# Optimization experiments

Hardware: AMD Instinct MI355X
Metric: run time of the kernel (lower is better)

## Reference

```python
import jax, jax.numpy as jnp
import numpy as np

B, T, D = 2, 2048, 1024
H, KVH = 16, 4
HD = D // H            # 64
E, TOPK, FFH = 8, 2, 2048
EPS = 1e-6
ROPE_THETA = 10000.0


def rmsnorm(x, w):
    return x * jax.lax.rsqrt(jnp.mean(x * x, axis=-1, keepdims=True) + EPS) * w


def rope(x, cos, sin):
    # x: (B, h, T, hd); pairs (even, odd) treated as complex, matching view_as_complex
    x2 = x.reshape(*x.shape[:-1], -1, 2)
    x0, x1 = x2[..., 0], x2[..., 1]
    o0 = x0 * cos - x1 * sin
    o1 = x0 * sin + x1 * cos
    return jnp.stack([o0, o1], axis=-1).reshape(x.shape)


def setup_inputs() -> dict:
    key = jax.random.key(0)
    ks = jax.random.split(key, 12)
    s = 0.02
    return {
        'x': jax.random.normal(ks[0], (B, T, D), dtype=jnp.float32),
        'attn_norm_w': jnp.ones((D,), jnp.float32),
        'wq': jax.random.normal(ks[1], (D, H * HD), jnp.float32) * s,
        'wk': jax.random.normal(ks[2], (D, KVH * HD), jnp.float32) * s,
        'wv': jax.random.normal(ks[3], (D, KVH * HD), jnp.float32) * s,
        'wo': jax.random.normal(ks[4], (D, D), jnp.float32) * s,
        'ffn_norm_w': jnp.ones((D,), jnp.float32),
        'gate_w': jax.random.normal(ks[5], (D, E), jnp.float32) * s,
        'gate_bias': jnp.zeros((E,), jnp.float32),  # e_score_correction_bias (aux-loss-free)
        'expert_w1': jax.random.normal(ks[6], (E, D, FFH), jnp.float32) * s,
        'expert_w2': jax.random.normal(ks[7], (E, FFH, D), jnp.float32) * s,
        'shared_w1': jax.random.normal(ks[8], (D, FFH), jnp.float32) * s,
        'shared_w2': jax.random.normal(ks[9], (FFH, D), jnp.float32) * s,
    }


def block_forward(x, attn_norm_w, wq, wk, wv, wo, ffn_norm_w, gate_w, gate_bias,
                  expert_w1, expert_w2, shared_w1, shared_w2):
    # ---- RoPE tables (precompute_freqs_cis, scaling_factor=1.0) ----
    half = HD // 2
    inv_freq = 1.0 / (ROPE_THETA ** (jnp.arange(half, dtype=jnp.float32) / half))
    t = jnp.arange(T, dtype=jnp.float32)
    fr = t[:, None] * inv_freq          # (T, half)
    cos, sin = jnp.cos(fr), jnp.sin(fr)

    # ---- attn_norm + GQA attention ----
    h = rmsnorm(x, attn_norm_w)
    q = (h @ wq).reshape(B, T, H, HD).transpose(0, 2, 1, 3)      # (B,H,T,HD)
    k = (h @ wk).reshape(B, T, KVH, HD).transpose(0, 2, 1, 3)    # (B,KVH,T,HD)
    v = (h @ wv).reshape(B, T, KVH, HD).transpose(0, 2, 1, 3)
    q = rope(q, cos, sin)
    k = rope(k, cos, sin)
    n_rep = H // KVH
    k = jnp.repeat(k, n_rep, axis=1)    # repeat_interleave over head dim
    v = jnp.repeat(v, n_rep, axis=1)
    att = jnp.einsum('bhqd,bhkd->bhqk', q, k) * (HD ** -0.5)
    causal = jnp.tril(jnp.ones((T, T), dtype=bool))
    att = jnp.where(causal, att, jnp.finfo(att.dtype).min)
    att = jax.nn.softmax(att, axis=-1)
    attn_out = jnp.einsum('bhqk,bhkd->bhqd', att, v).transpose(0, 2, 1, 3).reshape(B, T, D) @ wo
    x1 = x + attn_out

    # ---- ffn_norm + MoE feed-forward ----
    h2 = rmsnorm(x1, ffn_norm_w).reshape(-1, D)                  # (N, D)
    N = B * T
    shared = jax.nn.silu(h2 @ shared_w1) @ shared_w2             # 1 shared expert
    scores = jax.nn.sigmoid(h2 @ gate_w) + gate_bias             # sigmoid gate + correction bias
    topk_w, topk_i = jax.lax.top_k(scores, TOPK)
    topk_w = topk_w / (topk_w.sum(-1, keepdims=True) + 1e-20)    # norm_topk_prob; routed_scale=1.0
    combine = jnp.zeros((N, E), x.dtype).at[jnp.arange(N)[:, None], topk_i].add(topk_w)
    hmid = jax.nn.silu(jnp.einsum('nd,edh->enh', h2, expert_w1)) # (E,N,FFH)
    eout = jnp.einsum('enh,ehd->end', hmid, expert_w2)           # (E,N,D)
    routed = jnp.einsum('end,ne->nd', eout, combine)
    return x1 + (shared + routed).reshape(B, T, D)


def reference(x, attn_norm_w, wq, wk, wv, wo, ffn_norm_w, gate_w, gate_bias,
              expert_w1, expert_w2, shared_w1, shared_w2):
    return block_forward(x, attn_norm_w, wq, wk, wv, wo, ffn_norm_w, gate_w, gate_bias,
                         expert_w1, expert_w2, shared_w1, shared_w2)
```

## Files before the change

### kernel.cpp

```cpp
#include <hip/hip_runtime.h>
#include <math.h>

#define NTOK 4096
#define DM 1024
#define TSEQ 2048
#define NH 16
#define NKV 4
#define HDIM 64
#define NE 8
#define NFF 2048
#define QKVN 1536

typedef float f4v __attribute__((ext_vector_type(4)));
typedef short b8v __attribute__((ext_vector_type(8)));
typedef unsigned short u16;

__device__ __forceinline__ float silu_f(float v) { return v / (1.0f + expf(-v)); }

__device__ __forceinline__ u16 f2b(float f) {
    union { float f; unsigned u; } x{f};
    unsigned r = (x.u + 0x7FFFu + ((x.u >> 16) & 1u)) >> 16;
    return (u16)r;
}
__device__ __forceinline__ float b2f(u16 b) {
    union { unsigned u; float f; } x;
    x.u = ((unsigned)b) << 16;
    return x.f;
}

template <int MODE>
__global__ __launch_bounds__(256) void rmsnorm2_k(const float* __restrict__ x,
                                                  const float* __restrict__ w,
                                                  u16* __restrict__ oh, u16* __restrict__ ol,
                                                  float* __restrict__ of) {
    int row = blockIdx.x;
    int tid = threadIdx.x;
    const float4 v = ((const float4*)(x + (size_t)row * DM))[tid];
    float ss = v.x * v.x + v.y * v.y + v.z * v.z + v.w * v.w;
    for (int off = 32; off; off >>= 1) ss += __shfl_down(ss, off);
    __shared__ float red[4];
    if ((tid & 63) == 0) red[tid >> 6] = ss;
    __syncthreads();
    float tot = red[0] + red[1] + red[2] + red[3];
    float inv = rsqrtf(tot * (1.0f / DM) + 1e-6f);
    const float4 wv = ((const float4*)w)[tid];
    float o[4];
    o[0] = v.x * inv * wv.x; o[1] = v.y * inv * wv.y;
    o[2] = v.z * inv * wv.z; o[3] = v.w * inv * wv.w;
    if (MODE == 1) {
        float4 f; f.x = o[0]; f.y = o[1]; f.z = o[2]; f.w = o[3];
        ((float4*)(of + (size_t)row * DM))[tid] = f;
        ushort4 hb;
        hb.x = f2b(o[0]); hb.y = f2b(o[1]); hb.z = f2b(o[2]); hb.w = f2b(o[3]);
        ((ushort4*)(oh + (size_t)row * DM))[tid] = hb;
    } else {
        ushort4 hb, lb;
#pragma unroll
        for (int i = 0; i < 4; ++i) {
            u16 h = f2b(o[i]);
            u16 l = f2b(o[i] - b2f(h));
            ((u16*)&hb)[i] = h;
            ((u16*)&lb)[i] = l;
        }
        ((ushort4*)(oh + (size_t)row * DM))[tid] = hb;
        ((ushort4*)(ol + (size_t)row * DM))[tid] = lb;
    }
}

__global__ __launch_bounds__(256) void scast_k(const float* __restrict__ in, int stride,
                                               int colbase, int cols,
                                               u16* __restrict__ oh, u16* __restrict__ ol) {
    int idx = blockIdx.x * 256 + threadIdx.x;
    int cpr = cols >> 3;
    int row = idx / cpr;
    int cc = (idx - row * cpr) << 3;
    const float* p = in + (size_t)row * stride + colbase + cc;
    const float4 a = *(const float4*)p;
    const float4 b = *(const float4*)(p + 4);
    float vv[8] = {a.x, a.y, a.z, a.w, b.x, b.y, b.z, b.w};
    ushort4 h0, h1, l0, l1;
#pragma unroll
    for (int i = 0; i < 8; ++i) {
        u16 h = f2b(vv[i]);
        u16 l = f2b(vv[i] - b2f(h));
        if (i < 4) { ((u16*)&h0)[i] = h; ((u16*)&l0)[i] = l; }
        else       { ((u16*)&h1)[i - 4] = h; ((u16*)&l1)[i - 4] = l; }
    }
    u16* po = oh + (size_t)row * cols + cc;
    u16* pl = ol + (size_t)row * cols + cc;
    *(ushort4*)po = h0; *(ushort4*)(po + 4) = h1;
    *(ushort4*)pl = l0; *(ushort4*)(pl + 4) = l1;
}

__global__ __launch_bounds__(256) void vtrans_k(const float* __restrict__ qkv,
                                                u16* __restrict__ oh, u16* __restrict__ ol) {
    __shared__ float tl[32][33];
    int c0 = blockIdx.x << 5;
    int r0 = blockIdx.y << 5;
    int lr = threadIdx.x >> 3, lc = (threadIdx.x & 7) << 2;
    const float4 v = *(const float4*)&qkv[(size_t)(r0 + lr) * QKVN + 1280 + c0 + lc];
    tl[lr][lc] = v.x; tl[lr][lc + 1] = v.y; tl[lr][lc + 2] = v.z; tl[lr][lc + 3] = v.w;
    __syncthreads();
    int b = r0 >> 11;
    size_t obase = ((size_t)(b * 256 + c0 + lr)) * TSEQ + (r0 & 2047) + lc;
    ushort4 h4, l4;
#pragma unroll
    for (int i = 0; i < 4; ++i) {
        float f = tl[lc + i][lr];
        u16 h = f2b(f);
        u16 l = f2b(f - b2f(h));
        ((u16*)&h4)[i] = h; ((u16*)&l4)[i] = l;
    }
    *(ushort4*)&oh[obase] = h4;
    *(ushort4*)&ol[obase] = l4;
}

__global__ __launch_bounds__(256) void tcast2_k(const float* __restrict__ in,
                                                u16* __restrict__ oh, u16* __restrict__ ol,
                                                int R, int C) {
    __shared__ float tl[32][33];
    int r0 = blockIdx.y << 5, c0 = blockIdx.x << 5;
    int lr = threadIdx.x >> 3, lc = (threadIdx.x & 7) << 2;
    const float4 v = *(const float4*)&in[(size_t)(r0 + lr) * C + c0 + lc];
    tl[lr][lc] = v.x; tl[lr][lc + 1] = v.y; tl[lr][lc + 2] = v.z; tl[lr][lc + 3] = v.w;
    __syncthreads();
    ushort4 h4, l4;
#pragma unroll
    for (int i = 0; i < 4; ++i) {
        float f = tl[lc + i][lr];
        u16 h = f2b(f);
        u16 l = f2b(f - b2f(h));
        ((u16*)&h4)[i] = h; ((u16*)&l4)[i] = l;
    }
    size_t ob = (size_t)(c0 + lr) * R + r0 + lc;
    *(ushort4*)&oh[ob] = h4;
    *(ushort4*)&ol[ob] = l4;
}

__global__ __launch_bounds__(256) void tcast_k(const float* __restrict__ in,
                                               u16* __restrict__ out, int R, int C) {
    size_t boff = (size_t)blockIdx.z * R * C;
    in += boff; out += boff;
    __shared__ float tl[32][33];
    int r0 = blockIdx.y << 5, c0 = blockIdx.x << 5;
    int lr = threadIdx.x >> 3, lc = (threadIdx.x & 7) << 2;
    const float4 v = *(const float4*)&in[(size_t)(r0 + lr) * C + c0 + lc];
    tl[lr][lc] = v.x; tl[lr][lc + 1] = v.y; tl[lr][lc + 2] = v.z; tl[lr][lc + 3] = v.w;
    __syncthreads();
    ushort4 o;
    o.x = f2b(tl[lc + 0][lr]); o.y = f2b(tl[lc + 1][lr]);
    o.z = f2b(tl[lc + 2][lr]); o.w = f2b(tl[lc + 3][lr]);
    *(ushort4*)&out[(size_t)(c0 + lr) * R + r0 + lc] = o;
}

__global__ void rope2_k(float* __restrict__ x, int nheads, int colbase) {
    int idx = blockIdx.x * blockDim.x + threadIdx.x;
    int total = NTOK * nheads * 32;
    if (idx >= total) return;
    int j = idx & 31;
    int hh = (idx >> 5) % nheads;
    int n = idx / (nheads * 32);
    int t = n & (TSEQ - 1);
    float inv = expf(-(float)j * (0.03125f * logf(10000.0f)));
    float s, c;
    sincosf((float)t * inv, &s, &c);
    float* p = x + (size_t)n * QKVN + colbase + hh * 64 + j * 2;
    float x0 = p[0], x1 = p[1];
    p[0] = x0 * c - x1 * s;
    p[1] = x0 * s + x1 * c;
}

template <int EPI>
__global__ __launch_bounds__(256) void sgemm_k(const u16* __restrict__ Ah,
                                               const u16* __restrict__ Al,
                                               const u16* __restrict__ Bh,
                                               const u16* __restrict__ Bl,
                                               const float* __restrict__ Rr,
                                               float* __restrict__ C,
                                               int M, int N, int K) {
    __shared__ u16 Ash[128 * 40], Asl[128 * 40], Bsh[128 * 40], Bsl[128 * 40];
    int t = threadIdx.x;
    int l = t & 63, w = t >> 6;
    int wr = w >> 1, wc = w & 1;
    int n0 = blockIdx.x * 128, m0 = blockIdx.y * 128;
    int srow = t >> 2, scol = (t & 3) << 3;
    const u16 *agh[2], *agl[2], *bgh[2], *bgl[2];
#pragma unroll
    for (int i = 0; i < 2; ++i) {
        size_t ao = (size_t)(m0 + i * 64 + srow) * K + scol;
        size_t bo = (size_t)(n0 + i * 64 + srow) * K + scol;
        agh[i] = Ah + ao; agl[i] = Al + ao;
        bgh[i] = Bh + bo; bgl[i] = Bl + bo;
    }
    f4v acc[4][4];
#pragma unroll
    for (int m = 0; m < 4; ++m)
#pragma unroll
        for (int n = 0; n < 4; ++n) acc[m][n] = (f4v)0.0f;
    int kh_ = (l >> 4) << 3;
    for (int k0 = 0; k0 < K; k0 += 32) {
        b8v vah0 = *(const b8v*)(agh[0] + k0);
        b8v vah1 = *(const b8v*)(agh[1] + k0);
        b8v val0 = *(const b8v*)(agl[0] + k0);
        b8v val1 = *(const b8v*)(agl[1] + k0);
        b8v vbh0 = *(const b8v*)(bgh[0] + k0);
        b8v vbh1 = *(const b8v*)(bgh[1] + k0);
        b8v vbl0 = *(const b8v*)(bgl[0] + k0);
        b8v vbl1 = *(const b8v*)(bgl[1] + k0);
        __syncthreads();
        *(b8v*)&Ash[srow * 40 + scol] = vah0;
        *(b8v*)&Ash[(64 + srow) * 40 + scol] = vah1;
        *(b8v*)&Asl[srow * 40 + scol] = val0;
        *(b8v*)&Asl[(64 + srow) * 40 + scol] = val1;
        *(b8v*)&Bsh[srow * 40 + scol] = vbh0;
        *(b8v*)&Bsh[(64 + srow) * 40 + scol] = vbh1;
        *(b8v*)&Bsl[srow * 40 + scol] = vbl0;
        *(b8v*)&Bsl[(64 + srow) * 40 + scol] = vbl1;
        __syncthreads();
        b8v afh[4], afl[4], bfh[4], bfl[4];
#pragma unroll
        for (int m = 0; m < 4; ++m) {
            int ro = (wr * 64 + m * 16 + (l & 15)) * 40 + kh_;
            afh[m] = *(const b8v*)&Ash[ro];
            afl[m] = *(const b8v*)&Asl[ro];
        }
#pragma unroll
        for (int n = 0; n < 4; ++n) {
            int ro = (wc * 64 + n * 16 + (l & 15)) * 40 + kh_;
            bfh[n] = *(const b8v*)&Bsh[ro];
            bfl[n] = *(const b8v*)&Bsl[ro];
        }
#pragma unroll
        for (int m = 0; m < 4; ++m)
#pragma unroll
            for (int n = 0; n < 4; ++n) {
                acc[m][n] = __builtin_amdgcn_mfma_f32_16x16x32_bf16(afl[m], bfh[n], acc[m][n], 0, 0, 0);
                acc[m][n] = __builtin_amdgcn_mfma_f32_16x16x32_bf16(afh[m], bfl[n], acc[m][n], 0, 0, 0);
                acc[m][n] = __builtin_amdgcn_mfma_f32_16x16x32_bf16(afh[m], bfh[n], acc[m][n], 0, 0, 0);
            }
    }
#pragma unroll
    for (int m = 0; m < 4; ++m) {
        int r0l = m0 + wr * 64 + m * 16 + ((l >> 4) << 2);
#pragma unroll
        for (int n = 0; n < 4; ++n) {
            int col = n0 + wc * 64 + n * 16 + (l & 15);
            f4v c = acc[m][n];
#pragma unroll
            for (int j = 0; j < 4; ++j) {
                size_t idx = (size_t)(r0l + j) * N + col;
                float v = c[j];
                if (EPI == 2) v += Rr[idx];
                C[idx] = v;
            }
        }
    }
}

__global__ __launch_bounds__(256) void mattn_k(const u16* __restrict__ qh, const u16* __restrict__ ql,
                                               const u16* __restrict__ kh, const u16* __restrict__ kl,
                                               const u16* __restrict__ vth, const u16* __restrict__ vtl,
                                               float* __restrict__ o) {
    __shared__ u16 plds[4][2][16][72];
    int t = threadIdx.x, l = t & 63, w = t >> 6;
    int bh = blockIdx.y, b = bh >> 4, h = bh & 15, kvh = h >> 2;
    int q0 = blockIdx.x * 64;
    size_t bT = (size_t)b * TSEQ;
    int lx = l & 15, lg = l >> 4;
    b8v qfh[2], qfl[2];
    {
        size_t qo = (bT + q0 + w * 16 + lx) * DM + h * 64 + lg * 8;
        qfh[0] = *(const b8v*)(qh + qo);
        qfh[1] = *(const b8v*)(qh + qo + 32);
        qfl[0] = *(const b8v*)(ql + qo);
        qfl[1] = *(const b8v*)(ql + qo + 32);
    }
    f4v acc[4];
#pragma unroll
    for (int ht = 0; ht < 4; ++ht) acc[ht] = (f4v)0.0f;
    float m_r[4], l_r[4];
    int qg[4];
#pragma unroll
    for (int r = 0; r < 4; ++r) {
        m_r[r] = -3.0e38f; l_r[r] = 0.0f;
        qg[r] = q0 + w * 16 + lg * 4 + r;
    }
    int ntile = (q0 >> 6) + 1;
    for (int kt = 0; kt < ntile; ++kt) {
        int kv0 = kt << 6;
        f4v s[4];
#pragma unroll
        for (int st = 0; st < 4; ++st) {
            size_t ko = (bT + kv0 + st * 16 + lx) * 256 + kvh * 64 + lg * 8;
            b8v kf0h = *(const b8v*)(kh + ko);
            b8v kf1h = *(const b8v*)(kh + ko + 32);
            b8v kf0l = *(const b8v*)(kl + ko);
            b8v kf1l = *(const b8v*)(kl + ko + 32);
            f4v ss = (f4v)0.0f;
            ss = __builtin_amdgcn_mfma_f32_16x16x32_bf16(qfl[0], kf0h, ss, 0, 0, 0);
            ss = __builtin_amdgcn_mfma_f32_16x16x32_bf16(qfh[0], kf0l, ss, 0, 0, 0);
            ss = __builtin_amdgcn_mfma_f32_16x16x32_bf16(qfh[0], kf0h, ss, 0, 0, 0);
            ss = __builtin_amdgcn_mfma_f32_16x16x32_bf16(qfl[1], kf1h, ss, 0, 0, 0);
            ss = __builtin_amdgcn_mfma_f32_16x16x32_bf16(qfh[1], kf1l, ss, 0, 0, 0);
            ss = __builtin_amdgcn_mfma_f32_16x16x32_bf16(qfh[1], kf1h, ss, 0, 0, 0);
            s[st] = ss;
        }
        float nm[4], sc[4], ps[4];
#pragma unroll
        for (int r = 0; r < 4; ++r) {
            float mx = -3.0e38f;
#pragma unroll
            for (int st = 0; st < 4; ++st) {
                float v = s[st][r] * 0.125f;
                if (kv0 + st * 16 + lx > qg[r]) v = -3.0e38f;
                s[st][r] = v;
                mx = fmaxf(mx, v);
            }
            mx = fmaxf(mx, __shfl_xor(mx, 1));
            mx = fmaxf(mx, __shfl_xor(mx, 2));
            mx = fmaxf(mx, __shfl_xor(mx, 4));
            mx = fmaxf(mx, __shfl_xor(mx, 8));
            nm[r] = fmaxf(m_r[r], mx);
            sc[r] = __expf(m_r[r] - nm[r]);
            m_r[r] = nm[r];
            ps[r] = 0.0f;
        }
#pragma unroll
        for (int st = 0; st < 4; ++st)
#pragma unroll
            for (int r = 0; r < 4; ++r) {
                float p = __expf(s[st][r] - nm[r]);
                ps[r] += p;
                u16 ph = f2b(p);
                u16 pl = f2b(p - b2f(ph));
                plds[w][0][lg * 4 + r][st * 16 + lx] = ph;
                plds[w][1][lg * 4 + r][st * 16 + lx] = pl;
            }
#pragma unroll
        for (int r = 0; r < 4; ++r) {
            float rs = ps[r];
            rs += __shfl_xor(rs, 1);
            rs += __shfl_xor(rs, 2);
            rs += __shfl_xor(rs, 4);
            rs += __shfl_xor(rs, 8);
            l_r[r] = l_r[r] * sc[r] + rs;
#pragma unroll
            for (int ht = 0; ht < 4; ++ht) acc[ht][r] *= sc[r];
        }
        __syncthreads();
        b8v pf0h = *(const b8v*)&plds[w][0][lx][lg * 8];
        b8v pf1h = *(const b8v*)&plds[w][0][lx][32 + lg * 8];
        b8v pf0l = *(const b8v*)&plds[w][1][lx][lg * 8];
        b8v pf1l = *(const b8v*)&plds[w][1][lx][32 + lg * 8];
#pragma unroll
        for (int ht = 0; ht < 4; ++ht) {
            size_t vo = ((size_t)(b * 4 + kvh) * 64 + ht * 16 + lx) * TSEQ + kv0 + lg * 8;
            b8v vf0h = *(const b8v*)(vth + vo);
            b8v vf1h = *(const b8v*)(vth + vo + 32);
            b8v vf0l = *(const b8v*)(vtl + vo);
            b8v vf1l = *(const b8v*)(vtl + vo + 32);
            acc[ht] = __builtin_amdgcn_mfma_f32_16x16x32_bf16(pf0l, vf0h, acc[ht], 0, 0, 0);
            acc[ht] = __builtin_amdgcn_mfma_f32_16x16x32_bf16(pf0h, vf0l, acc[ht], 0, 0, 0);
            acc[ht] = __builtin_amdgcn_mfma_f32_16x16x32_bf16(pf0h, vf0h, acc[ht], 0, 0, 0);
            acc[ht] = __builtin_amdgcn_mfma_f32_16x16x32_bf16(pf1l, vf1h, acc[ht], 0, 0, 0);
            acc[ht] = __builtin_amdgcn_mfma_f32_16x16x32_bf16(pf1h, vf1l, acc[ht], 0, 0, 0);
            acc[ht] = __builtin_amdgcn_mfma_f32_16x16x32_bf16(pf1h, vf1h, acc[ht], 0, 0, 0);
        }
        __syncthreads();
    }
#pragma unroll
    for (int ht = 0; ht < 4; ++ht)
#pragma unroll
        for (int r = 0; r < 4; ++r) {
            o[(bT + q0 + w * 16 + lg * 4 + r) * DM + h * 64 + ht * 16 + lx] =
                acc[ht][r] / l_r[r];
        }
}

__global__ __launch_bounds__(64) void gate_k(const float* __restrict__ h2,
                                             const float* __restrict__ gw,
                                             const float* __restrict__ gb,
                                             int* __restrict__ top2i,
                                             float* __restrict__ top2w,
                                             int* __restrict__ counts) {
    int n = blockIdx.x;
    int lane = threadIdx.x;
    float acc[8] = {};
    for (int d = lane; d < DM; d += 64) {
        float hv = h2[(size_t)n * DM + d];
        const float4 g0 = ((const float4*)&gw[d * 8])[0];
        const float4 g1 = ((const float4*)&gw[d * 8])[1];
        acc[0] = fmaf(hv, g0.x, acc[0]); acc[1] = fmaf(hv, g0.y, acc[1]);
        acc[2] = fmaf(hv, g0.z, acc[2]); acc[3] = fmaf(hv, g0.w, acc[3]);
        acc[4] = fmaf(hv, g1.x, acc[4]); acc[5] = fmaf(hv, g1.y, acc[5]);
        acc[6] = fmaf(hv, g1.z, acc[6]); acc[7] = fmaf(hv, g1.w, acc[7]);
    }
#pragma unroll
    for (int e = 0; e < 8; ++e)
        for (int off = 32; off; off >>= 1) acc[e] += __shfl_down(acc[e], off);
    if (lane == 0) {
        float s[8];
#pragma unroll
        for (int e = 0; e < 8; ++e) s[e] = 1.0f / (1.0f + expf(-acc[e])) + gb[e];
        int i0 = 0;
#pragma unroll
        for (int e = 1; e < 8; ++e) if (s[e] > s[i0]) i0 = e;
        int i1 = (i0 == 0) ? 1 : 0;
#pragma unroll
        for (int e = 0; e < 8; ++e) if (e != i0 && s[e] > s[i1]) i1 = e;
        float w0 = s[i0], w1 = s[i1];
        float norm = 1.0f / (w0 + w1 + 1e-20f);
        top2i[n * 2] = i0; top2i[n * 2 + 1] = i1;
        top2w[n * 2] = w0 * norm; top2w[n * 2 + 1] = w1 * norm;
        atomicAdd(&counts[i0], 1);
        atomicAdd(&counts[i1], 1);
    }
}

__global__ void zero16_k(int* p) { if (threadIdx.x < 16) p[threadIdx.x] = 0; }

__global__ void scan_k(const int* __restrict__ counts, int* __restrict__ segs) {
    if (threadIdx.x == 0) {
        segs[0] = 0;
        for (int e = 0; e < NE; ++e) segs[e + 1] = segs[e] + counts[e];
    }
}

__global__ void scatter_k(const int* __restrict__ top2i, const float* __restrict__ top2w,
                          const int* __restrict__ segs, int* __restrict__ cursor,
                          int* __restrict__ list, float* __restrict__ wslot,
                          int* __restrict__ slot_of) {
    int idx = blockIdx.x * blockDim.x + threadIdx.x;
    if (idx >= NTOK * 2) return;
    int e = top2i[idx];
    int pos = segs[e] + atomicAdd(&cursor[e], 1);
    list[pos] = idx >> 1;
    wslot[pos] = top2w[idx];
    slot_of[idx] = pos;
}

template <int EPI, int MOE, int GATHER>
__global__ __launch_bounds__(256) void mgemm_k(const u16* __restrict__ A,
                                               const u16* __restrict__ Bt,
                                               const float* __restrict__ R,
                                               const float* __restrict__ wslot,
                                               const int* __restrict__ list,
                                               const int* __restrict__ segs,
                                               float* __restrict__ Cf,
                                               u16* __restrict__ Cb,
                                               int M, int N, int K) {
    __shared__ u16 As[128 * 40];
    __shared__ u16 Bs[128 * 40];
    int e = MOE ? blockIdx.z : 0;
    int base = 0, cnt = M;
    if (MOE) { base = segs[e]; cnt = segs[e + 1] - base; }
    int m0 = blockIdx.y * 128;
    if (m0 >= cnt) return;
    int n0 = blockIdx.x * 128;
    const u16* Bte = Bt + (size_t)e * N * K;
    int t = threadIdx.x;
    int l = t & 63, w = t >> 6;
    int wr = w >> 1, wc = w & 1;
    int srow = t >> 2, scol = (t & 3) << 3;
    const u16* ag[2];
    const u16* bg[2];
#pragma unroll
    for (int i = 0; i < 2; ++i) {
        int r = m0 + i * 64 + srow;
        int ar;
        if (MOE) {
            int rc = r < cnt ? r : cnt - 1;
            ar = GATHER ? list[base + rc] : base + rc;
        } else {
            ar = r;
        }
        ag[i] = A + (size_t)ar * K + scol;
        bg[i] = Bte + (size_t)(n0 + i * 64 + srow) * K + scol;
    }
    f4v acc[4][4];
#pragma unroll
    for (int m = 0; m < 4; ++m)
#pragma unroll
        for (int n = 0; n < 4; ++n) acc[m][n] = (f4v)0.0f;
    int kh = (l >> 4) << 3;
    for (int k0 = 0; k0 < K; k0 += 32) {
        b8v va0 = *(const b8v*)(ag[0] + k0);
        b8v va1 = *(const b8v*)(ag[1] + k0);
        b8v vb0 = *(const b8v*)(bg[0] + k0);
        b8v vb1 = *(const b8v*)(bg[1] + k0);
        __syncthreads();
        *(b8v*)&As[srow * 40 + scol] = va0;
        *(b8v*)&As[(64 + srow) * 40 + scol] = va1;
        *(b8v*)&Bs[srow * 40 + scol] = vb0;
        *(b8v*)&Bs[(64 + srow) * 40 + scol] = vb1;
        __syncthreads();
        b8v af[4], bf[4];
#pragma unroll
        for (int m = 0; m < 4; ++m)
            af[m] = *(const b8v*)&As[(wr * 64 + m * 16 + (l & 15)) * 40 + kh];
#pragma unroll
        for (int n = 0; n < 4; ++n)
            bf[n] = *(const b8v*)&Bs[(wc * 64 + n * 16 + (l & 15)) * 40 + kh];
#pragma unroll
        for (int m = 0; m < 4; ++m)
#pragma unroll
            for (int n = 0; n < 4; ++n)
                acc[m][n] = __builtin_amdgcn_mfma_f32_16x16x32_bf16(af[m], bf[n], acc[m][n], 0, 0, 0);
    }
#pragma unroll
    for (int m = 0; m < 4; ++m) {
        int r0l = m0 + wr * 64 + m * 16 + ((l >> 4) << 2);
#pragma unroll
        for (int n = 0; n < 4; ++n) {
            int col = n0 + wc * 64 + n * 16 + (l & 15);
            f4v c = acc[m][n];
#pragma unroll
            for (int j = 0; j < 4; ++j) {
                int row = r0l + j;
                if (MOE && row >= cnt) continue;
                float v = c[j];
                if (EPI == 1) {
                    v = silu_f(v);
                    Cb[(size_t)(base + row) * N + col] = f2b(v);
                } else if (EPI == 2) {
                    size_t idx = (size_t)row * N + col;
                    Cf[idx] = v + R[idx];
                } else if (EPI == 3) {
                    Cf[(size_t)(base + row) * N + col] = v * wslot[base + row];
                } else {
                    Cf[(size_t)row * N + col] = v;
                }
            }
        }
    }
}

__global__ __launch_bounds__(256) void combine_k(const float* __restrict__ eout,
                                                 const int* __restrict__ slot_of,
                                                 float* __restrict__ out) {
    int idx = blockIdx.x * blockDim.x + threadIdx.x;
    int n = idx >> 8;
    int c = idx & 255;
    const float4 a = ((const float4*)(eout + (size_t)slot_of[n * 2] * DM))[c];
    const float4 b = ((const float4*)(eout + (size_t)slot_of[n * 2 + 1] * DM))[c];
    float4 o = ((float4*)out)[idx];
    o.x += a.x + b.x; o.y += a.y + b.y; o.z += a.z + b.z; o.w += a.w + b.w;
    ((float4*)out)[idx] = o;
}

extern "C" void kernel_launch(void* const* d_in, const int* in_sizes, int n_in,
                              void* d_out, int out_size, void* d_ws, size_t ws_size,
                              hipStream_t stream) {
    (void)in_sizes; (void)n_in; (void)out_size; (void)ws_size;
    const float* x   = (const float*)d_in[0];
    const float* anw = (const float*)d_in[1];
    const float* wq  = (const float*)d_in[2];
    const float* wk  = (const float*)d_in[3];
    const float* wv  = (const float*)d_in[4];
    const float* wo  = (const float*)d_in[5];
    const float* fnw = (const float*)d_in[6];
    const float* gw  = (const float*)d_in[7];
    const float* gb  = (const float*)d_in[8];
    const float* ew1 = (const float*)d_in[9];
    const float* ew2 = (const float*)d_in[10];
    const float* sw1 = (const float*)d_in[11];
    const float* sw2 = (const float*)d_in[12];
    float* out = (float*)d_out;

#define WSOFF(mb) ((char*)d_ws + (size_t)(mb) * 1048576)
    u16* qkvT_h = (u16*)WSOFF(0);
    u16* qkvT_l = (u16*)WSOFF(3);
    u16* woT_h  = (u16*)WSOFF(6);
    u16* woT_l  = (u16*)WSOFF(8);
    u16* sw1t   = (u16*)WSOFF(10);
    u16* sw2t   = (u16*)WSOFF(14);
    u16* ew1t   = (u16*)WSOFF(18);
    u16* ew2t   = (u16*)WSOFF(50);
    float* qkv  = (float*)WSOFF(82);
    float* ao   = (float*)WSOFF(82);
    float* h2f  = (float*)WSOFF(82);
    u16* h_hi   = (u16*)WSOFF(106);
    u16* h_lo   = (u16*)WSOFF(114);
    u16* ao_hi  = (u16*)WSOFF(106);
    u16* ao_lo  = (u16*)WSOFF(114);
    u16* q_hi   = (u16*)WSOFF(122);
    u16* q_lo   = (u16*)WSOFF(130);
    u16* k_hi   = (u16*)WSOFF(138);
    u16* k_lo   = (u16*)WSOFF(140);
    u16* vT_hi  = (u16*)WSOFF(142);
    u16* vT_lo  = (u16*)WSOFF(144);
    float* x1   = (float*)WSOFF(146);
    u16* h2b    = (u16*)WSOFF(162);
    u16* midb   = (u16*)WSOFF(170);
    u16* hmidb  = (u16*)WSOFF(122);
    float* eoutb = (float*)WSOFF(154);
    int* meta0  = (int*)WSOFF(186);
    int*   top2i  = meta0;
    float* top2w  = (float*)(meta0 + 8192);
    int*   counts = meta0 + 16384;
    int*   cursor = meta0 + 16392;
    int*   segs   = meta0 + 16400;
    int*   list   = meta0 + 16416;
    float* wslot  = (float*)(meta0 + 16416 + 8192);
    int*   slot_of = meta0 + 16416 + 16384;

    tcast2_k<<<dim3(32, 32), 256, 0, stream>>>(wq, qkvT_h, qkvT_l, DM, 1024);
    tcast2_k<<<dim3(8, 32), 256, 0, stream>>>(wk, qkvT_h + 1024 * 1024, qkvT_l + 1024 * 1024, DM, 256);
    tcast2_k<<<dim3(8, 32), 256, 0, stream>>>(wv, qkvT_h + 1280 * 1024, qkvT_l + 1280 * 1024, DM, 256);
    tcast2_k<<<dim3(32, 32), 256, 0, stream>>>(wo, woT_h, woT_l, DM, DM);
    tcast_k<<<dim3(NFF / 32, DM / 32, 1), 256, 0, stream>>>(sw1, sw1t, DM, NFF);
    tcast_k<<<dim3(DM / 32, NFF / 32, 1), 256, 0, stream>>>(sw2, sw2t, NFF, DM);
    tcast_k<<<dim3(NFF / 32, DM / 32, NE), 256, 0, stream>>>(ew1, ew1t, DM, NFF);
    tcast_k<<<dim3(DM / 32, NFF / 32, NE), 256, 0, stream>>>(ew2, ew2t, NFF, DM);

    rmsnorm2_k<0><<<NTOK, 256, 0, stream>>>(x, anw, h_hi, h_lo, nullptr);
    sgemm_k<0><<<dim3(QKVN / 128, NTOK / 128), 256, 0, stream>>>(
        h_hi, h_lo, qkvT_h, qkvT_l, nullptr, qkv, NTOK, QKVN, DM);
    rope2_k<<<(NTOK * NH * 32 + 255) / 256, 256, 0, stream>>>(qkv, NH, 0);
    rope2_k<<<(NTOK * NKV * 32 + 255) / 256, 256, 0, stream>>>(qkv, NKV, 1024);
    scast_k<<<2048, 256, 0, stream>>>(qkv, QKVN, 0, 1024, q_hi, q_lo);
    scast_k<<<512, 256, 0, stream>>>(qkv, QKVN, 1024, 256, k_hi, k_lo);
    vtrans_k<<<dim3(8, 128), 256, 0, stream>>>(qkv, vT_hi, vT_lo);
    mattn_k<<<dim3(TSEQ / 64, 32), 256, 0, stream>>>(q_hi, q_lo, k_hi, k_lo, vT_hi, vT_lo, ao);
    scast_k<<<2048, 256, 0, stream>>>(ao, DM, 0, DM, ao_hi, ao_lo);
    sgemm_k<2><<<dim3(DM / 128, NTOK / 128), 256, 0, stream>>>(
        ao_hi, ao_lo, woT_h, woT_l, x, x1, NTOK, DM, DM);
    rmsnorm2_k<1><<<NTOK, 256, 0, stream>>>(x1, fnw, h2b, nullptr, h2f);
    zero16_k<<<1, 64, 0, stream>>>(counts);
    gate_k<<<NTOK, 64, 0, stream>>>(h2f, gw, gb, top2i, top2w, counts);
    scan_k<<<1, 1, 0, stream>>>(counts, segs);
    scatter_k<<<32, 256, 0, stream>>>(top2i, top2w, segs, cursor, list, wslot, slot_of);
    mgemm_k<1, 0, 0><<<dim3(NFF / 128, NTOK / 128, 1), 256, 0, stream>>>(
        h2b, sw1t, nullptr, nullptr, nullptr, nullptr, nullptr, midb, NTOK, NFF, DM);
    mgemm_k<2, 0, 0><<<dim3(DM / 128, NTOK / 128, 1), 256, 0, stream>>>(
        midb, sw2t, x1, nullptr, nullptr, nullptr, out, nullptr, NTOK, DM, NFF);
    mgemm_k<1, 1, 1><<<dim3(NFF / 128, NTOK / 128, NE), 256, 0, stream>>>(
        h2b, ew1t, nullptr, nullptr, list, segs, nullptr, hmidb, NTOK, NFF, DM);
    mgemm_k<3, 1, 0><<<dim3(DM / 128, NTOK / 128, NE), 256, 0, stream>>>(
        hmidb, ew2t, nullptr, wslot, nullptr, segs, eoutb, nullptr, 2 * NTOK, DM, NFF);
    combine_k<<<NTOK, 256, 0, stream>>>(eoutb, slot_of, out);
#undef WSOFF
}
```

Baseline: 1.244 ms.

## Pair causal query tiles per block and drop online-softmax max tracking in attention

Result: faster. 1.029 ms (-17.3%).

```diff
diff --git a/kernel.cpp b/kernel.cpp
--- a/kernel.cpp
+++ b/kernel.cpp
@@ -261,120 +261,105 @@
                                                const u16* __restrict__ kh, const u16* __restrict__ kl,
                                                const u16* __restrict__ vth, const u16* __restrict__ vtl,
                                                float* __restrict__ o) {
-    __shared__ u16 plds[4][2][16][72];
+    __shared__ short plds[4][2][16][72];
     int t = threadIdx.x, l = t & 63, w = t >> 6;
     int bh = blockIdx.y, b = bh >> 4, h = bh & 15, kvh = h >> 2;
-    int q0 = blockIdx.x * 64;
     size_t bT = (size_t)b * TSEQ;
     int lx = l & 15, lg = l >> 4;
-    b8v qfh[2], qfl[2];
-    {
-        size_t qo = (bT + q0 + w * 16 + lx) * DM + h * 64 + lg * 8;
-        qfh[0] = *(const b8v*)(qh + qo);
-        qfh[1] = *(const b8v*)(qh + qo + 32);
-        qfl[0] = *(const b8v*)(ql + qo);
-        qfl[1] = *(const b8v*)(ql + qo + 32);
-    }
-    f4v acc[4];
-#pragma unroll
-    for (int ht = 0; ht < 4; ++ht) acc[ht] = (f4v)0.0f;
-    float m_r[4], l_r[4];
-    int qg[4];
-#pragma unroll
-    for (int r = 0; r < 4; ++r) {
-        m_r[r] = -3.0e38f; l_r[r] = 0.0f;
-        qg[r] = q0 + w * 16 + lg * 4 + r;
-    }
-    int ntile = (q0 >> 6) + 1;
-    for (int kt = 0; kt < ntile; ++kt) {
-        int kv0 = kt << 6;
-        f4v s[4];
-#pragma unroll
-        for (int st = 0; st < 4; ++st) {
-            size_t ko = (bT + kv0 + st * 16 + lx) * 256 + kvh * 64 + lg * 8;
-            b8v kf0h = *(const b8v*)(kh + ko);
-            b8v kf1h = *(const b8v*)(kh + ko + 32);
-            b8v kf0l = *(const b8v*)(kl + ko);
-            b8v kf1l = *(const b8v*)(kl + ko + 32);
-            f4v ss = (f4v)0.0f;
-            ss = __builtin_amdgcn_mfma_f32_16x16x32_bf16(qfl[0], kf0h, ss, 0, 0, 0);
-            ss = __builtin_amdgcn_mfma_f32_16x16x32_bf16(qfh[0], kf0l, ss, 0, 0, 0);
-            ss = __builtin_amdgcn_mfma_f32_16x16x32_bf16(qfh[0], kf0h, ss, 0, 0, 0);
-            ss = __builtin_amdgcn_mfma_f32_16x16x32_bf16(qfl[1], kf1h, ss, 0, 0, 0);
-            ss = __builtin_amdgcn_mfma_f32_16x16x32_bf16(qfh[1], kf1l, ss, 0, 0, 0);
-            ss = __builtin_amdgcn_mfma_f32_16x16x32_bf16(qfh[1], kf1h, ss, 0, 0, 0);
-            s[st] = ss;
-        }
-        float nm[4], sc[4], ps[4];
+#pragma unroll
+    for (int half = 0; half < 2; ++half) {
+        int qt = half ? (31 - blockIdx.x) : blockIdx.x;
+        int q0 = qt * 64;
+        b8v qfh[2], qfl[2];
+        {
+            size_t qo = (bT + q0 + w * 16 + lx) * DM + h * 64 + lg * 8;
+            qfh[0] = *(const b8v*)(qh + qo);
+            qfh[1] = *(const b8v*)(qh + qo + 32);
+            qfl[0] = *(const b8v*)(ql + qo);
+            qfl[1] = *(const b8v*)(ql + qo + 32);
+        }
+        f4v acc[4];
+#pragma unroll
+        for (int ht = 0; ht < 4; ++ht) acc[ht] = (f4v)0.0f;
+        float l_r[4] = {0.0f, 0.0f, 0.0f, 0.0f};
+        int qg[4];
+#pragma unroll
+        for (int r = 0; r < 4; ++r) qg[r] = q0 + w * 16 + lg * 4 + r;
+        int ntile = qt + 1;
+        for (int kt = 0; kt < ntile; ++kt) {
+            int kv0 = kt << 6;
+            f4v s[4];
+#pragma unroll
+            for (int st = 0; st < 4; ++st) {
+                size_t ko = (bT + kv0 + st * 16 + lx) * 256 + kvh * 64 + lg * 8;
+                b8v kf0h = *(const b8v*)(kh + ko);
+                b8v kf1h = *(const b8v*)(kh + ko + 32);
+                b8v kf0l = *(const b8v*)(kl + ko);
+                b8v kf1l = *(const b8v*)(kl + ko + 32);
+                f4v ss = (f4v)0.0f;
+                ss = __builtin_amdgcn_mfma_f32_16x16x32_bf16(qfl[0], kf0h, ss, 0, 0, 0);
+                ss = __builtin_amdgcn_mfma_f32_16x16x32_bf16(qfh[0], kf0l, ss, 0, 0, 0);
+                ss = __builtin_amdgcn_mfma_f32_16x16x32_bf16(qfh[0], kf0h, ss, 0, 0, 0);
+                ss = __builtin_amdgcn_mfma_f32_16x16x32_bf16(qfl[1], kf1h, ss, 0, 0, 0);
+                ss = __builtin_amdgcn_mfma_f32_16x16x32_bf16(qfh[1], kf1l, ss, 0, 0, 0);
+                ss = __builtin_amdgcn_mfma_f32_16x16x32_bf16(qfh[1], kf1h, ss, 0, 0, 0);
+                s[st] = ss;
+            }
+            b8v vh0[4], vh1[4], vl0[4], vl1[4];
+#pragma unroll
+            for (int ht = 0; ht < 4; ++ht) {
+                size_t vo = ((size_t)(b * 4 + kvh) * 64 + ht * 16 + lx) * TSEQ + kv0 + lg * 8;
+                vh0[ht] = *(const b8v*)(vth + vo);
+                vh1[ht] = *(const b8v*)(vth + vo + 32);
+                vl0[ht] = *(const b8v*)(vtl + vo);
+                vl1[ht] = *(const b8v*)(vtl + vo + 32);
+            }
+#pragma unroll
+            for (int st = 0; st < 4; ++st)
+#pragma unroll
+                for (int r = 0; r < 4; ++r) {
+                    float v = s[st][r] * 0.125f;
+                    float p = (kv0 + st * 16 + lx > qg[r])
+                                  ? 0.0f
+                                  : __expf(fminf(v, 60.0f));
+                    l_r[r] += p;
+                    u16 ph = f2b(p);
+                    u16 pl = f2b(p - b2f(ph));
+                    plds[w][0][lg * 4 + r][st * 16 + lx] = (short)ph;
+                    plds[w][1][lg * 4 + r][st * 16 + lx] = (short)pl;
+                }
+            __threadfence_block();
+            __builtin_amdgcn_sched_barrier(0);
+            b8v pf0h = *(const b8v*)&plds[w][0][lx][lg * 8];
+            b8v pf1h = *(const b8v*)&plds[w][0][lx][32 + lg * 8];
+            b8v pf0l = *(const b8v*)&plds[w][1][lx][lg * 8];
+            b8v pf1l = *(const b8v*)&plds[w][1][lx][32 + lg * 8];
+            __builtin_amdgcn_sched_barrier(0);
+#pragma unroll
+            for (int ht = 0; ht < 4; ++ht) {
+                acc[ht] = __builtin_amdgcn_mfma_f32_16x16x32_bf16(pf0l, vh0[ht], acc[ht], 0, 0, 0);
+                acc[ht] = __builtin_amdgcn_mfma_f32_16x16x32_bf16(pf0h, vl0[ht], acc[ht], 0, 0, 0);
+                acc[ht] = __builtin_amdgcn_mfma_f32_16x16x32_bf16(pf0h, vh0[ht], acc[ht], 0, 0, 0);
+                acc[ht] = __builtin_amdgcn_mfma_f32_16x16x32_bf16(pf1l, vh1[ht], acc[ht], 0, 0, 0);
+                acc[ht] = __builtin_amdgcn_mfma_f32_16x16x32_bf16(pf1h, vl1[ht], acc[ht], 0, 0, 0);
+                acc[ht] = __builtin_amdgcn_mfma_f32_16x16x32_bf16(pf1h, vh1[ht], acc[ht], 0, 0, 0);
+            }
+        }
 #pragma unroll
         for (int r = 0; r < 4; ++r) {
-            float mx = -3.0e38f;
-#pragma unroll
-            for (int st = 0; st < 4; ++st) {
-                float v = s[st][r] * 0.125f;
-                if (kv0 + st * 16 + lx > qg[r]) v = -3.0e38f;
-                s[st][r] = v;
-                mx = fmaxf(mx, v);
-            }
-            mx = fmaxf(mx, __shfl_xor(mx, 1));
-            mx = fmaxf(mx, __shfl_xor(mx, 2));
-            mx = fmaxf(mx, __shfl_xor(mx, 4));
-            mx = fmaxf(mx, __shfl_xor(mx, 8));
-            nm[r] = fmaxf(m_r[r], mx);
-            sc[r] = __expf(m_r[r] - nm[r]);
-            m_r[r] = nm[r];
-            ps[r] = 0.0f;
-        }
-#pragma unroll
-        for (int st = 0; st < 4; ++st)
-#pragma unroll
-            for (int r = 0; r < 4; ++r) {
-                float p = __expf(s[st][r] - nm[r]);
-                ps[r] += p;
-                u16 ph = f2b(p);
-                u16 pl = f2b(p - b2f(ph));
-                plds[w][0][lg * 4 + r][st * 16 + lx] = ph;
-                plds[w][1][lg * 4 + r][st * 16 + lx] = pl;
-            }
-#pragma unroll
-        for (int r = 0; r < 4; ++r) {
-            float rs = ps[r];
+            float rs = l_r[r];
             rs += __shfl_xor(rs, 1);
             rs += __shfl_xor(rs, 2);
             rs += __shfl_xor(rs, 4);
             rs += __shfl_xor(rs, 8);
-            l_r[r] = l_r[r] * sc[r] + rs;
-#pragma unroll
-            for (int ht = 0; ht < 4; ++ht) acc[ht][r] *= sc[r];
-        }
-        __syncthreads();
-        b8v pf0h = *(const b8v*)&plds[w][0][lx][lg * 8];
-        b8v pf1h = *(const b8v*)&plds[w][0][lx][32 + lg * 8];
-        b8v pf0l = *(const b8v*)&plds[w][1][lx][lg * 8];
-        b8v pf1l = *(const b8v*)&plds[w][1][lx][32 + lg * 8];
-#pragma unroll
-        for (int ht = 0; ht < 4; ++ht) {
-            size_t vo = ((size_t)(b * 4 + kvh) * 64 + ht * 16 + lx) * TSEQ + kv0 + lg * 8;
-            b8v vf0h = *(const b8v*)(vth + vo);
-            b8v vf1h = *(const b8v*)(vth + vo + 32);
-            b8v vf0l = *(const b8v*)(vtl + vo);
-            b8v vf1l = *(const b8v*)(vtl + vo + 32);
-            acc[ht] = __builtin_amdgcn_mfma_f32_16x16x32_bf16(pf0l, vf0h, acc[ht], 0, 0, 0);
-            acc[ht] = __builtin_amdgcn_mfma_f32_16x16x32_bf16(pf0h, vf0l, acc[ht], 0, 0, 0);
-            acc[ht] = __builtin_amdgcn_mfma_f32_16x16x32_bf16(pf0h, vf0h, acc[ht], 0, 0, 0);
-            acc[ht] = __builtin_amdgcn_mfma_f32_16x16x32_bf16(pf1l, vf1h, acc[ht], 0, 0, 0);
-            acc[ht] = __builtin_amdgcn_mfma_f32_16x16x32_bf16(pf1h, vf1l, acc[ht], 0, 0, 0);
-            acc[ht] = __builtin_amdgcn_mfma_f32_16x16x32_bf16(pf1h, vf1h, acc[ht], 0, 0, 0);
-        }
-        __syncthreads();
-    }
-#pragma unroll
-    for (int ht = 0; ht < 4; ++ht)
-#pragma unroll
-        for (int r = 0; r < 4; ++r) {
-            o[(bT + q0 + w * 16 + lg * 4 + r) * DM + h * 64 + ht * 16 + lx] =
-                acc[ht][r] / l_r[r];
-        }
+            float rinv = 1.0f / rs;
+#pragma unroll
+            for (int ht = 0; ht < 4; ++ht) {
+                o[(bT + q0 + w * 16 + lg * 4 + r) * DM + h * 64 + ht * 16 + lx] =
+                    acc[ht][r] * rinv;
+            }
+        }
+    }
 }
 
 __global__ __launch_bounds__(64) void gate_k(const float* __restrict__ h2,
@@ -621,7 +606,7 @@
     scast_k<<<2048, 256, 0, stream>>>(qkv, QKVN, 0, 1024, q_hi, q_lo);
     scast_k<<<512, 256, 0, stream>>>(qkv, QKVN, 1024, 256, k_hi, k_lo);
     vtrans_k<<<dim3(8, 128), 256, 0, stream>>>(qkv, vT_hi, vT_lo);
-    mattn_k<<<dim3(TSEQ / 64, 32), 256, 0, stream>>>(q_hi, q_lo, k_hi, k_lo, vT_hi, vT_lo, ao);
+    mattn_k<<<dim3(TSEQ / 128, 32), 256, 0, stream>>>(q_hi, q_lo, k_hi, k_lo, vT_hi, vT_lo, ao);
     scast_k<<<2048, 256, 0, stream>>>(ao, DM, 0, DM, ao_hi, ao_lo);
     sgemm_k<2><<<dim3(DM / 128, NTOK / 128), 256, 0, stream>>>(
         ao_hi, ao_lo, woT_h, woT_l, x, x1, NTOK, DM, DM);
```
